# Optimization experiments

Measured on AMD Instinct MI355X. Metric: run time of the kernel, lower is better.

The kernel has to match this reference:

```python
import jax, jax.numpy as jnp
import numpy as np

NUM_HEADS = 6
KERNEL = 5
EPS = 1e-6


def _neighbor_idx(L, k):
    # NATTEN neighborhood: window start clamped so every query has exactly k neighbors
    starts = jnp.clip(jnp.arange(L) - k // 2, 0, L - k)
    return starts[:, None] + jnp.arange(k)  # [L, k]


def ada_rmsnorm(x, scale, w1, b1, w2, b2):
    # x: [B,C,D,H,W]; RMS over spatial dims, gamma from channel means via small MLP
    rms = jnp.sqrt(jnp.mean(x * x, axis=(2, 3, 4), keepdims=True) + EPS)
    xn = x / rms
    stats = jnp.mean(x, axis=(2, 3, 4))                 # [B,C]
    h = jax.nn.relu(stats @ w1.T + b1)                  # [B,2C]
    gamma = jax.nn.sigmoid(h @ w2.T + b2)               # [B,C]
    return xn * (scale * gamma[:, :, None, None, None])


def reference(x, scale1, n1_w1, n1_b1, n1_w2, n1_b2,
              qkv_w, qkv_b, proj_w, proj_b,
              scale2, n2_w1, n2_b1, n2_w2, n2_b2,
              mlp_w1, mlp_b1, mlp_w2, mlp_b2):
    B, C, D, H, W = x.shape
    nh_, k_ = NUM_HEADS, KERNEL
    hd = C // nh_
    K3 = k_ ** 3

    # --- norm1 + neighborhood attention ---
    h = ada_rmsnorm(x, scale1, n1_w1, n1_b1, n1_w2, n1_b2)
    t = jnp.transpose(h, (0, 2, 3, 4, 1))               # [B,D,H,W,C]
    qkv = t @ qkv_w.T + qkv_b                           # [B,D,H,W,3C]
    q, k, v = jnp.split(qkv, 3, axis=-1)
    q = q.reshape(B, D, H, W, nh_, hd)
    k = k.reshape(B, D, H, W, nh_, hd)
    v = v.reshape(B, D, H, W, nh_, hd)

    iD = _neighbor_idx(D, k_)
    iH = _neighbor_idx(H, k_)
    iW = _neighbor_idx(W, k_)
    nd = iD[:, None, None, :, None, None]               # [D,1,1,k,1,1]
    nhh = iH[None, :, None, None, :, None]              # [1,H,1,1,k,1]
    nw = iW[None, None, :, None, None, :]               # [1,1,W,1,1,k]

    k_nb = k[:, nd, nhh, nw].reshape(B, D, H, W, K3, nh_, hd)
    v_nb = v[:, nd, nhh, nw].reshape(B, D, H, W, K3, nh_, hd)

    scale_qk = hd ** -0.5
    scores = jnp.einsum('bdhwnc,bdhwknc->bdhwnk', q, k_nb) * scale_qk  # [B,D,H,W,heads,K3]
    p = jax.nn.softmax(scores, axis=-1)
    o = jnp.einsum('bdhwnk,bdhwknc->bdhwnc', p, v_nb).reshape(B, D, H, W, C)
    o = o @ proj_w.T + proj_b                            # output projection
    x = x + jnp.transpose(o, (0, 4, 1, 2, 3))

    # --- norm2 + 1x1-conv MLP (GELU exact) ---
    h2 = ada_rmsnorm(x, scale2, n2_w1, n2_b1, n2_w2, n2_b2)
    m = jnp.einsum('oc,bcdhw->bodhw', mlp_w1, h2) + mlp_b1[None, :, None, None, None]
    m = jax.nn.gelu(m, approximate=False)
    m = jnp.einsum('oc,bcdhw->bodhw', mlp_w2, m) + mlp_b2[None, :, None, None, None]
    return x + m


def setup_inputs() -> dict:
    key = jax.random.key(0)
    ks = jax.random.split(key, 16)
    B, C, D, H, W = 1, 192, 16, 16, 16
    hid = 2 * C
    mlp_h = int(4.0 * C)
    s = 0.02
    inp = {
        'x': jax.random.normal(ks[0], (B, C, D, H, W), jnp.float32),
        'scale1': jnp.ones((1, C, 1, 1, 1), jnp.float32),
        'n1_w1': jax.random.normal(ks[1], (hid, C), jnp.float32) * s,
        'n1_b1': jnp.zeros((hid,), jnp.float32),
        'n1_w2': jax.random.normal(ks[2], (C, hid), jnp.float32) * s,
        'n1_b2': jnp.zeros((C,), jnp.float32),
        'qkv_w': jax.random.normal(ks[3], (3 * C, C), jnp.float32) * s,
        'qkv_b': jnp.zeros((3 * C,), jnp.float32),
        'proj_w': jax.random.normal(ks[4], (C, C), jnp.float32) * s,
        'proj_b': jnp.zeros((C,), jnp.float32),
        'scale2': jnp.ones((1, C, 1, 1, 1), jnp.float32),
        'n2_w1': jax.random.normal(ks[5], (hid, C), jnp.float32) * s,
        'n2_b1': jnp.zeros((hid,), jnp.float32),
        'n2_w2': jax.random.normal(ks[6], (C, hid), jnp.float32) * s,
        'n2_b2': jnp.zeros((C,), jnp.float32),
        'mlp_w1': jax.random.normal(ks[7], (mlp_h, C), jnp.float32) * s,
        'mlp_b1': jnp.zeros((mlp_h,), jnp.float32),
        'mlp_w2': jax.random.normal(ks[8], (C, mlp_h), jnp.float32) * s,
        'mlp_b2': jnp.zeros((C,), jnp.float32),
    }
    return inp
```

## Files before the change

### kernel.cpp

```cpp
#include <hip/hip_runtime.h>
#include <hip/hip_bf16.h>
#include <cmath>


#define NPOS 4096
#define C_CH 192
#define NB   512

typedef __bf16 bf16x8 __attribute__((ext_vector_type(8)));
typedef __bf16 bf16x4 __attribute__((ext_vector_type(4)));
typedef float  f32x4  __attribute__((ext_vector_type(4)));

__device__ __forceinline__ void pre_sync(unsigned* bar, int grp) {
    __syncthreads();
    if (threadIdx.x == 0) {
        unsigned* arr    = bar + 128 + grp * 16;
        unsigned* master = bar + 256;
        unsigned* go     = bar + 272 + grp * 16;
        unsigned prev = __hip_atomic_fetch_add(arr, 1u, __ATOMIC_RELAXED,
                                               __HIP_MEMORY_SCOPE_AGENT);
        if (prev == 63u) {
            __hip_atomic_fetch_add(master, 1u, __ATOMIC_RELAXED,
                                   __HIP_MEMORY_SCOPE_AGENT);
            while (__hip_atomic_load(master, __ATOMIC_RELAXED,
                                     __HIP_MEMORY_SCOPE_AGENT) < 8u)
                __builtin_amdgcn_s_sleep(2);
            __hip_atomic_store(go, 1u, __ATOMIC_RELAXED, __HIP_MEMORY_SCOPE_AGENT);
        }
        while (__hip_atomic_load(go, __ATOMIC_RELAXED,
                                 __HIP_MEMORY_SCOPE_AGENT) == 0u)
            __builtin_amdgcn_s_sleep(2);
    }
    __syncthreads();
}

__device__ __forceinline__ void grid_sync(unsigned* bar, int idx, int xcc,
                                          unsigned myPop, unsigned nx) {
    __syncthreads();
    if (threadIdx.x == 0) {
        unsigned* base   = bar + 512 + idx * 512;
        unsigned* arr    = base + xcc * 16;
        unsigned* master = base + 128;
        unsigned* go     = base + 144 + xcc * 16;
        unsigned prev = __hip_atomic_fetch_add(arr, 1u, __ATOMIC_RELAXED,
                                               __HIP_MEMORY_SCOPE_AGENT);
        if (prev == myPop - 1u) {
            __hip_atomic_fetch_add(master, 1u, __ATOMIC_RELEASE,
                                   __HIP_MEMORY_SCOPE_AGENT);
            while (__hip_atomic_load(master, __ATOMIC_RELAXED,
                                     __HIP_MEMORY_SCOPE_AGENT) < nx)
                __builtin_amdgcn_s_sleep(2);
            __hip_atomic_store(go, 1u, __ATOMIC_RELAXED, __HIP_MEMORY_SCOPE_AGENT);
        }
        while (__hip_atomic_load(go, __ATOMIC_RELAXED,
                                 __HIP_MEMORY_SCOPE_AGENT) == 0u)
            __builtin_amdgcn_s_sleep(2);
    }
    __syncthreads();
}

__device__ __forceinline__ void conv_unit(const float* __restrict__ src,
                                          __bf16* __restrict__ dst, int base)
{
    int i = (base * 256 + (int)threadIdx.x) * 4;
    float4 v = *(const float4*)(src + i);
    bf16x4 o = { (__bf16)v.x, (__bf16)v.y, (__bf16)v.z, (__bf16)v.w };
    *(bf16x4*)(dst + i) = o;
}

__device__ void stats_unit(float* sm, const float* __restrict__ x,
                           float* __restrict__ sums, float* __restrict__ sumsq, int c)
{
    const float4* xc = (const float4*)(x + (size_t)c * NPOS);
    float a = 0.f, a2 = 0.f;
    for (int i = threadIdx.x; i < NPOS / 4; i += 256) {
        float4 v = xc[i];
        a  += v.x + v.y + v.z + v.w;
        a2 += v.x * v.x + v.y * v.y + v.z * v.z + v.w * v.w;
    }
    #pragma unroll
    for (int off = 32; off > 0; off >>= 1) {
        a  += __shfl_down(a, off);
        a2 += __shfl_down(a2, off);
    }
    float* ls = sm; float* ls2 = sm + 4;
    int wid = threadIdx.x >> 6;
    if ((threadIdx.x & 63) == 0) { ls[wid] = a; ls2[wid] = a2; }
    __syncthreads();
    if (threadIdx.x == 0) {
        float t = 0.f, t2 = 0.f;
        #pragma unroll
        for (int w = 0; w < 4; w++) { t += ls[w]; t2 += ls2[w]; }
        sums[c] = t; sumsq[c] = t2;
    }
    __syncthreads();
}

__device__ void transpose_unit(float* sm, const float* __restrict__ x,
                               __bf16* __restrict__ xb, int p0)
{
    float* lds = sm;
    int t = threadIdx.x;
    for (int idx = t; idx < 192 * 4; idx += 256) {
        int row = idx >> 2, p4 = idx & 3;
        float4 v = *(const float4*)(x + (size_t)row * NPOS + p0 + p4 * 4);
        lds[row * 17 + p4 * 4 + 0] = v.x;
        lds[row * 17 + p4 * 4 + 1] = v.y;
        lds[row * 17 + p4 * 4 + 2] = v.z;
        lds[row * 17 + p4 * 4 + 3] = v.w;
    }
    __syncthreads();
    for (int idx = t; idx < 48 * 16; idx += 256) {
        int c4 = idx >> 4, p = idx & 15;
        bf16x4 o;
        #pragma unroll
        for (int j = 0; j < 4; j++) o[j] = (__bf16)lds[(c4 * 4 + j) * 17 + p];
        *(bf16x4*)(xb + (size_t)(p0 + p) * 192 + c4 * 4) = o;
    }
    __syncthreads();
}

__device__ void compute_gsl(float* scratch, float* gslOut,
    const float* __restrict__ sums, const float* __restrict__ sumsq,
    const float* __restrict__ scale,
    const __bf16* __restrict__ w1b, const float* __restrict__ b1,
    const __bf16* __restrict__ w2b, const float* __restrict__ b2)
{
    float* stats = scratch;
    float* h     = scratch + 192;
    int t = threadIdx.x;
    if (t < C_CH)
        stats[t] = __hip_atomic_load((const float*)&sums[t], __ATOMIC_RELAXED,
                                     __HIP_MEMORY_SCOPE_AGENT) * (1.0f / (float)NPOS);
    __syncthreads();
    for (int j = t; j < 384; j += 256) {
        float acc = b1[j];
        const __bf16* wr = w1b + (size_t)j * C_CH;
        #pragma unroll 4
        for (int c = 0; c < C_CH; c += 8) {
            bf16x8 w8 = *(const bf16x8*)(wr + c);
            acc += (float)w8[0] * stats[c]     + (float)w8[1] * stats[c + 1]
                 + (float)w8[2] * stats[c + 2] + (float)w8[3] * stats[c + 3]
                 + (float)w8[4] * stats[c + 4] + (float)w8[5] * stats[c + 5]
                 + (float)w8[6] * stats[c + 6] + (float)w8[7] * stats[c + 7];
        }
        h[j] = fmaxf(acc, 0.0f);
    }
    __syncthreads();
    if (t < C_CH) {
        float acc = b2[t];
        const __bf16* wr = w2b + (size_t)t * 384;
        #pragma unroll 4
        for (int j = 0; j < 384; j += 8) {
            bf16x8 w8 = *(const bf16x8*)(wr + j);
            acc += (float)w8[0] * h[j]     + (float)w8[1] * h[j + 1]
                 + (float)w8[2] * h[j + 2] + (float)w8[3] * h[j + 3]
                 + (float)w8[4] * h[j + 4] + (float)w8[5] * h[j + 5]
                 + (float)w8[6] * h[j + 6] + (float)w8[7] * h[j + 7];
        }
        float g = 1.0f / (1.0f + __expf(-acc));
        float sq = __hip_atomic_load((const float*)&sumsq[t], __ATOMIC_RELAXED,
                                     __HIP_MEMORY_SCOPE_AGENT);
        float rms = sqrtf(sq * (1.0f / (float)NPOS) + 1e-6f);
        gslOut[t] = scale[t] * g / rms;
    }
    __syncthreads();
}

template <int K, int EPI, bool SCALEA>
__device__ void gemm_tile(__bf16* al, __bf16* bl, const float* gslLds,
    int bx, int by,
    const __bf16* __restrict__ W, const float* __restrict__ bias,
    const __bf16* __restrict__ X, void* __restrict__ out,
    const float* __restrict__ resid, int M, __bf16* __restrict__ out_kv,
    float* __restrict__ s2sum, float* __restrict__ s2sq,
    __bf16* __restrict__ xb2o)
{
    constexpr int KC  = 192;
    constexpr int LDA = 200;
    int t    = threadIdx.x;
    int lane = t & 63;
    int wv   = t >> 6;
    int r16  = lane & 15;
    int quad = lane >> 4;
    int wvm  = wv >> 1;
    int wvn  = wv & 1;
    int mBase = by * 64;
    int nBase = bx * 64;

    f32x4 acc[2][2];
    #pragma unroll
    for (int i = 0; i < 2; i++)
        #pragma unroll
        for (int j = 0; j < 2; j++)
            acc[i][j] = (f32x4){0.f, 0.f, 0.f, 0.f};

    for (int k0 = 0; k0 < K; k0 += KC) {
        #pragma unroll
        for (int it = 0; it < 6; it++) {
            int c = it * 256 + t;
            int row = c / 24, off = c - row * 24;
            bf16x8 va = *(const bf16x8*)(W + (size_t)(mBase + row) * K + k0 + off * 8);
            if (SCALEA) {
                #pragma unroll
                for (int j = 0; j < 8; j++)
                    va[j] = (__bf16)((float)va[j] * gslLds[off * 8 + j]);
            }
            *(bf16x8*)(al + row * LDA + off * 8) = va;
            bf16x8 vb = *(const bf16x8*)(X + (size_t)(nBase + row) * K + k0 + off * 8);
            *(bf16x8*)(bl + row * LDA + off * 8) = vb;
        }
        __syncthreads();
        #pragma unroll
        for (int ks = 0; ks < KC / 32; ks++) {
            bf16x8 a0 = *(const bf16x8*)(al + (wvm * 32 + r16) * LDA + ks * 32 + quad * 8);
            bf16x8 a1 = *(const bf16x8*)(al + (wvm * 32 + 16 + r16) * LDA + ks * 32 + quad * 8);
            bf16x8 b0 = *(const bf16x8*)(bl + (wvn * 32 + r16) * LDA + ks * 32 + quad * 8);
            bf16x8 b1 = *(const bf16x8*)(bl + (wvn * 32 + 16 + r16) * LDA + ks * 32 + quad * 8);
            acc[0][0] = __builtin_amdgcn_mfma_f32_16x16x32_bf16(a0, b0, acc[0][0], 0, 0, 0);
            acc[0][1] = __builtin_amdgcn_mfma_f32_16x16x32_bf16(a0, b1, acc[0][1], 0, 0, 0);
            acc[1][0] = __builtin_amdgcn_mfma_f32_16x16x32_bf16(a1, b0, acc[1][0], 0, 0, 0);
            acc[1][1] = __builtin_amdgcn_mfma_f32_16x16x32_bf16(a1, b1, acc[1][1], 0, 0, 0);
        }
        __syncthreads();
    }

    #pragma unroll
    for (int rt = 0; rt < 2; rt++) {
        int m0 = mBase + wvm * 32 + rt * 16 + quad * 4;
        float b0 = bias[m0], b1v = bias[m0 + 1], b2v = bias[m0 + 2], b3v = bias[m0 + 3];
        float ss[4] = {0.f, 0.f, 0.f, 0.f}, sq[4] = {0.f, 0.f, 0.f, 0.f};
        #pragma unroll
        for (int ct = 0; ct < 2; ct++) {
            int n = nBase + wvn * 32 + ct * 16 + r16;
            f32x4 a4 = acc[rt][ct];
            float g0 = a4[0] + b0, g1 = a4[1] + b1v, g2 = a4[2] + b2v, g3 = a4[3] + b3v;
            if (EPI == 0) {
                int sect = m0 / 192;
                int o0 = m0 - sect * 192;
                if (sect == 0) {
                    const float qs = 0.17677669529663687f;
                    *(float4*)((float*)out + (size_t)n * 192 + o0) =
                        make_float4(g0 * qs, g1 * qs, g2 * qs, g3 * qs);
                } else {
                    bf16x4 kvv = { (__bf16)g0, (__bf16)g1, (__bf16)g2, (__bf16)g3 };
                    *(bf16x4*)(out_kv + (size_t)n * 384 + (o0 >> 2) * 8 + (sect - 1) * 4) = kvv;
                }
            } else if (EPI == 2 || EPI == 4) {
                float* o = (float*)out;
                size_t i0 = (size_t)m0 * NPOS + n;
                float v0 = g0 + resid[i0];
                float v1 = g1 + resid[i0 + NPOS];
                float v2 = g2 + resid[i0 + 2 * NPOS];
                float v3 = g3 + resid[i0 + 3 * NPOS];
                o[i0] = v0; o[i0 + NPOS] = v1; o[i0 + 2 * NPOS] = v2; o[i0 + 3 * NPOS] = v3;
                if (EPI == 4) {
                    bf16x4 xv = { (__bf16)v0, (__bf16)v1, (__bf16)v2, (__bf16)v3 };
                    *(bf16x4*)(xb2o + (size_t)n * 192 + m0) = xv;
                    ss[0] += v0; sq[0] += v0 * v0;
                    ss[1] += v1; sq[1] += v1 * v1;
                    ss[2] += v2; sq[2] += v2 * v2;
                    ss[3] += v3; sq[3] += v3 * v3;
                }
            } else {
                bf16x4 v;
                v[0] = (__bf16)(0.5f * g0 * (1.0f + erff(g0 * 0.7071067811865475f)));
                v[1] = (__bf16)(0.5f * g1 * (1.0f + erff(g1 * 0.7071067811865475f)));
                v[2] = (__bf16)(0.5f * g2 * (1.0f + erff(g2 * 0.7071067811865475f)));
                v[3] = (__bf16)(0.5f * g3 * (1.0f + erff(g3 * 0.7071067811865475f)));
                *(bf16x4*)((__bf16*)out + (size_t)n * M + m0) = v;
            }
        }
        if (EPI == 4) {
            #pragma unroll
            for (int j = 0; j < 4; j++) {
                float s = ss[j], s2v = sq[j];
                #pragma unroll
                for (int off = 8; off >= 1; off >>= 1) {
                    s   += __shfl_down(s, off);
                    s2v += __shfl_down(s2v, off);
                }
                if (r16 == 0) {
                    atomicAdd(&s2sum[m0 + j], s);
                    atomicAdd(&s2sq[m0 + j], s2v);
                }
            }
        }
    }
}

__device__ void attn_mfma(char* smbase, const float* __restrict__ q,
                          const __bf16* __restrict__ kv, __bf16* __restrict__ o,
                          int pb, int head)
{
    __bf16* Qs = (__bf16*)smbase;
    __bf16* Ks = Qs + 64 * 40;
    __bf16* Vt = Ks + 128 * 40;
    __bf16* Ps = Vt + 32 * 136;

    int t = threadIdx.x;
    int wave = t >> 6, lane = t & 63, r16 = lane & 15, quad = lane >> 4;

    int Db = (pb >> 4) * 4, Hb = ((pb >> 2) & 3) * 4, Wb = (pb & 3) * 4;
    int r0d = min(max(Db - 2, 0), 8);
    int r0h = min(max(Hb - 2, 0), 8);
    int r0w = min(max(Wb - 2, 0), 8);

    for (int idx = t; idx < 512; idx += 256) {
        int qr = idx >> 3, c4 = (idx & 7) * 4;
        int pos = (Db + (qr >> 4)) * 256 + (Hb + ((qr >> 2) & 3)) * 16 + (Wb + (qr & 3));
        float4 v = *(const float4*)(q + (size_t)pos * 192 + head * 32 + c4);
        bf16x4 b = { (__bf16)v.x, (__bf16)v.y, (__bf16)v.z, (__bf16)v.w };
        *(bf16x4*)(Qs + qr * 40 + c4) = b;
    }

    int d0q = min(max(Db + wave - 2, 0), 11);
    int h0q = min(max(Hb + quad - 2, 0), 11);
    unsigned wm[4];
    #pragma unroll
    for (int reg = 0; reg < 4; reg++) {
        int w0q = min(max(Wb + reg - 2, 0), 11);
        unsigned m = 0;
        #pragma unroll
        for (int wk = 0; wk < 8; wk++) {
            int wa = r0w + wk;
            if (wa >= w0q && wa < w0q + 5) m |= (1u << wk);
        }
        wm[reg] = m;
    }

    float lpart[4] = {0.f, 0.f, 0.f, 0.f};
    f32x4 accO[2] = { (f32x4){0.f,0.f,0.f,0.f}, (f32x4){0.f,0.f,0.f,0.f} };
    int rowbase = wave * 16;

    for (int c = 0; c < 4; c++) {
        __syncthreads();
        for (int idx = t; idx < 1024; idx += 256) {
            int l128 = idx >> 3, cp = idx & 7;
            int pos = (r0d + c * 2 + (l128 >> 6)) * 256
                    + (r0h + ((l128 >> 3) & 7)) * 16 + (r0w + (l128 & 7));
            uint4 u = *(const uint4*)(kv + (size_t)pos * 384 + head * 64 + cp * 8);
            uint2 kk; kk.x = u.x; kk.y = u.y;
            *(uint2*)(Ks + l128 * 40 + cp * 4) = kk;
            unsigned short* vt0 = (unsigned short*)(Vt + (cp * 4) * 136 + l128);
            vt0[0]         = (unsigned short)(u.z & 0xffff);
            vt0[136]       = (unsigned short)(u.z >> 16);
            vt0[272]       = (unsigned short)(u.w & 0xffff);
            vt0[408]       = (unsigned short)(u.w >> 16);
        }
        __syncthreads();
        bf16x8 aq = *(const bf16x8*)(Qs + (rowbase + r16) * 40 + quad * 8);
        #pragma unroll
        for (int tn = 0; tn < 8; tn++) {
            bf16x8 bk = *(const bf16x8*)(Ks + (tn * 16 + r16) * 40 + quad * 8);
            f32x4 sc = __builtin_amdgcn_mfma_f32_16x16x32_bf16(
                           aq, bk, (f32x4){0.f,0.f,0.f,0.f}, 0, 0, 0);
            int local = tn * 16 + r16;
            int dka = r0d + c * 2 + (local >> 6);
            int hka = r0h + ((local >> 3) & 7);
            int wk  = local & 7;
            bool vdh = (dka >= d0q) && (dka < d0q + 5) &&
                       (hka >= h0q) && (hka < h0q + 5);
            #pragma unroll
            for (int reg = 0; reg < 4; reg++) {
                bool v = vdh && ((wm[reg] >> wk) & 1u);
                float p = v ? __expf(sc[reg]) : 0.f;
                lpart[reg] += p;
                Ps[(rowbase + quad * 4 + reg) * 136 + local] = (__bf16)p;
            }
        }
        __syncthreads();
        #pragma unroll
        for (int tn = 0; tn < 2; tn++) {
            #pragma unroll
            for (int ks = 0; ks < 4; ks++) {
                bf16x8 pa = *(const bf16x8*)(Ps + (rowbase + r16) * 136 + ks * 32 + quad * 8);
                bf16x8 bv = *(const bf16x8*)(Vt + (tn * 16 + r16) * 136 + ks * 32 + quad * 8);
                accO[tn] = __builtin_amdgcn_mfma_f32_16x16x32_bf16(pa, bv, accO[tn], 0, 0, 0);
            }
        }
    }

    #pragma unroll
    for (int reg = 0; reg < 4; reg++) {
        #pragma unroll
        for (int off = 1; off < 16; off <<= 1)
            lpart[reg] += __shfl_xor(lpart[reg], off);
    }
    #pragma unroll
    for (int tn = 0; tn < 2; tn++) {
        #pragma unroll
        for (int reg = 0; reg < 4; reg++) {
            int qr = rowbase + quad * 4 + reg;
            int pos = (Db + (qr >> 4)) * 256 + (Hb + ((qr >> 2) & 3)) * 16 + (Wb + (qr & 3));
            o[(size_t)pos * 192 + head * 32 + tn * 16 + r16] =
                (__bf16)(accO[tn][reg] / lpart[reg]);
        }
    }
}

__global__ __launch_bounds__(256) void fused(
    const float* __restrict__ x, const float* __restrict__ scale1,
    const float* __restrict__ n1_w1, const float* __restrict__ n1_b1,
    const float* __restrict__ n1_w2, const float* __restrict__ n1_b2,
    const float* __restrict__ qkv_w, const float* __restrict__ qkv_b,
    const float* __restrict__ proj_w, const float* __restrict__ proj_b,
    const float* __restrict__ scale2,
    const float* __restrict__ n2_w1, const float* __restrict__ n2_b1,
    const float* __restrict__ n2_w2, const float* __restrict__ n2_b2,
    const float* __restrict__ mlp_w1, const float* __restrict__ mlp_b1,
    const float* __restrict__ mlp_w2, const float* __restrict__ mlp_b2,
    float* __restrict__ ws, float* __restrict__ x2)
{
    __shared__ __align__(16) char smraw[52224];
    __bf16* al     = (__bf16*)smraw;
    __bf16* bl     = al + 64 * 200;
    float*  smf    = (float*)smraw;
    float*  gslLds = (float*)(smraw + 51200);

    float*  q_buf   = ws;
    __bf16* kv_buf  = (__bf16*)(ws + 786432);
    __bf16* xb      = (__bf16*)(ws + 2359296);
    __bf16* o_attn  = (__bf16*)(ws + 2752512);
    __bf16* qkv_wb  = (__bf16*)(ws + 3145728);
    __bf16* proj_wb = qkv_wb + 110592;
    __bf16* m1_wb   = proj_wb + 36864;
    __bf16* m2_wb   = m1_wb + 147456;
    float*  sums1   = ws + 3366912;
    float*  sumsq1  = ws + 3367104;
    float*  sums2   = ws + 3367296;
    float*  sumsq2  = ws + 3367488;
    __bf16* n1w1b   = (__bf16*)(ws + 3367680);
    __bf16* n1w2b   = n1w1b + 73728;
    __bf16* n2w1b   = n1w2b + 73728;
    __bf16* n2w2b   = n2w1b + 73728;
    unsigned* bar   = (unsigned*)(ws + 3515136);
    __bf16* m_buf   = (__bf16*)(ws + 3520512);
    __bf16* xb2     = (__bf16*)(ws + 5093376);

    int bid = blockIdx.x;
    int t   = threadIdx.x;

    int xcc = __builtin_amdgcn_s_getreg(63508) & 7;

    if (t == 0)
        __hip_atomic_fetch_add(bar + xcc * 16, 1u, __ATOMIC_RELAXED,
                               __HIP_MEMORY_SCOPE_AGENT);
    pre_sync(bar, bid & 7);
    unsigned myPop = 0, nx = 0;
    if (t == 0) {
        myPop = __hip_atomic_load(bar + xcc * 16, __ATOMIC_RELAXED,
                                  __HIP_MEMORY_SCOPE_AGENT);
        #pragma unroll
        for (int xi = 0; xi < 8; xi++)
            nx += (__hip_atomic_load(bar + xi * 16, __ATOMIC_RELAXED,
                                     __HIP_MEMORY_SCOPE_AGENT) > 0u) ? 1u : 0u;
    }

    for (int u = bid; u < 1169; u += NB) {
        if      (u < 108)  conv_unit(qkv_w,  qkv_wb, u);
        else if (u < 144)  conv_unit(proj_w, proj_wb, u - 108);
        else if (u < 288)  conv_unit(mlp_w1, m1_wb, u - 144);
        else if (u < 432)  conv_unit(mlp_w2, m2_wb, u - 288);
        else if (u < 504)  conv_unit(n1_w1,  n1w1b, u - 432);
        else if (u < 576)  conv_unit(n1_w2,  n1w2b, u - 504);
        else if (u < 648)  conv_unit(n2_w1,  n2w1b, u - 576);
        else if (u < 720)  conv_unit(n2_w2,  n2w2b, u - 648);
        else if (u < 912)  stats_unit(smf, x, sums1, sumsq1, u - 720);
        else if (u == 912) {
            if (t < 192) {
                __hip_atomic_store(&sums2[t], 0.f, __ATOMIC_RELAXED,
                                   __HIP_MEMORY_SCOPE_AGENT);
                __hip_atomic_store(&sumsq2[t], 0.f, __ATOMIC_RELAXED,
                                   __HIP_MEMORY_SCOPE_AGENT);
            }
        }
        else               transpose_unit(smf, x, xb, (u - 913) * 16);
    }
    grid_sync(bar, 0, xcc, myPop, nx);

    compute_gsl(smf, gslLds, sums1, sumsq1, scale1, n1w1b, n1_b1, n1w2b, n1_b2);
    for (int tile = bid; tile < 576; tile += NB)
        gemm_tile<192, 0, true>(al, bl, gslLds, tile & 63, tile >> 6,
                                qkv_wb, qkv_b, xb, (void*)q_buf,
                                nullptr, 576, kv_buf, nullptr, nullptr, nullptr);
    grid_sync(bar, 1, xcc, myPop, nx);

    if (bid < 384)
        attn_mfma(smraw, q_buf, kv_buf, o_attn, bid / 6, bid % 6);
    grid_sync(bar, 2, xcc, myPop, nx);

    if (bid < 192)
        gemm_tile<192, 4, false>(al, bl, nullptr, bid & 63, bid >> 6,
                                 proj_wb, proj_b, o_attn, (void*)x2,
                                 x, 192, nullptr, sums2, sumsq2, xb2);
    grid_sync(bar, 3, xcc, myPop, nx);

    compute_gsl(smf, gslLds, sums2, sumsq2, scale2, n2w1b, n2_b1, n2w2b, n2_b2);
    for (int tile = bid; tile < 768; tile += NB)
        gemm_tile<192, 3, true>(al, bl, gslLds, tile & 63, tile >> 6,
                                m1_wb, mlp_b1, xb2, (void*)m_buf,
                                nullptr, 768, nullptr, nullptr, nullptr, nullptr);
    grid_sync(bar, 4, xcc, myPop, nx);

    if (bid < 192)
        gemm_tile<768, 2, false>(al, bl, nullptr, bid & 63, bid >> 6,
                                 m2_wb, mlp_b2, m_buf, (void*)x2,
                                 x2, 192, nullptr, nullptr, nullptr, nullptr);
}

extern "C" void kernel_launch(void* const* d_in, const int* in_sizes, int n_in,
                              void* d_out, int out_size, void* d_ws, size_t ws_size,
                              hipStream_t stream)
{
    const float* x      = (const float*)d_in[0];
    const float* scale1 = (const float*)d_in[1];
    const float* n1_w1  = (const float*)d_in[2];
    const float* n1_b1  = (const float*)d_in[3];
    const float* n1_w2  = (const float*)d_in[4];
    const float* n1_b2  = (const float*)d_in[5];
    const float* qkv_w  = (const float*)d_in[6];
    const float* qkv_b  = (const float*)d_in[7];
    const float* proj_w = (const float*)d_in[8];
    const float* proj_b = (const float*)d_in[9];
    const float* scale2 = (const float*)d_in[10];
    const float* n2_w1  = (const float*)d_in[11];
    const float* n2_b1  = (const float*)d_in[12];
    const float* n2_w2  = (const float*)d_in[13];
    const float* n2_b2  = (const float*)d_in[14];
    const float* mlp_w1 = (const float*)d_in[15];
    const float* mlp_b1 = (const float*)d_in[16];
    const float* mlp_w2 = (const float*)d_in[17];
    const float* mlp_b2 = (const float*)d_in[18];

    float* ws = (float*)d_ws;
    float* x2 = (float*)d_out;

    hipMemsetAsync(ws + 3515136, 0, 3072 * sizeof(unsigned), stream);

    fused<<<NB, 256, 0, stream>>>(x, scale1, n1_w1, n1_b1, n1_w2, n1_b2,
                                  qkv_w, qkv_b, proj_w, proj_b,
                                  scale2, n2_w1, n2_b1, n2_w2, n2_b2,
                                  mlp_w1, mlp_b1, mlp_w2, mlp_b2,
                                  ws, x2);
}
```

Measured before the change: 192.8 us.

## Fuse RMS stats into transpose pass and grow persistent grid to 768 blocks

Result: slower. 213.5 us (+10.7%).

```diff
diff --git a/kernel.cpp b/kernel.cpp
--- a/kernel.cpp
+++ b/kernel.cpp
@@ -5,7 +5,7 @@
 
 #define NPOS 4096
 #define C_CH 192
-#define NB   512
+#define NB   768
 
 typedef __bf16 bf16x8 __attribute__((ext_vector_type(8)));
 typedef __bf16 bf16x4 __attribute__((ext_vector_type(4)));
@@ -19,7 +19,7 @@
         unsigned* go     = bar + 272 + grp * 16;
         unsigned prev = __hip_atomic_fetch_add(arr, 1u, __ATOMIC_RELAXED,
                                                __HIP_MEMORY_SCOPE_AGENT);
-        if (prev == 63u) {
+        if (prev == (NB / 8 - 1)) {
             __hip_atomic_fetch_add(master, 1u, __ATOMIC_RELAXED,
                                    __HIP_MEMORY_SCOPE_AGENT);
             while (__hip_atomic_load(master, __ATOMIC_RELAXED,
@@ -68,36 +68,10 @@
     *(bf16x4*)(dst + i) = o;
 }
 
-__device__ void stats_unit(float* sm, const float* __restrict__ x,
-                           float* __restrict__ sums, float* __restrict__ sumsq, int c)
-{
-    const float4* xc = (const float4*)(x + (size_t)c * NPOS);
-    float a = 0.f, a2 = 0.f;
-    for (int i = threadIdx.x; i < NPOS / 4; i += 256) {
-        float4 v = xc[i];
-        a  += v.x + v.y + v.z + v.w;
-        a2 += v.x * v.x + v.y * v.y + v.z * v.z + v.w * v.w;
-    }
-    #pragma unroll
-    for (int off = 32; off > 0; off >>= 1) {
-        a  += __shfl_down(a, off);
-        a2 += __shfl_down(a2, off);
-    }
-    float* ls = sm; float* ls2 = sm + 4;
-    int wid = threadIdx.x >> 6;
-    if ((threadIdx.x & 63) == 0) { ls[wid] = a; ls2[wid] = a2; }
-    __syncthreads();
-    if (threadIdx.x == 0) {
-        float t = 0.f, t2 = 0.f;
-        #pragma unroll
-        for (int w = 0; w < 4; w++) { t += ls[w]; t2 += ls2[w]; }
-        sums[c] = t; sumsq[c] = t2;
-    }
-    __syncthreads();
-}
-
-__device__ void transpose_unit(float* sm, const float* __restrict__ x,
-                               __bf16* __restrict__ xb, int p0)
+__device__ void transpose_stats_unit(float* sm, const float* __restrict__ x,
+                                     __bf16* __restrict__ xb, int p0,
+                                     float* __restrict__ sums,
+                                     float* __restrict__ sumsq)
 {
     float* lds = sm;
     int t = threadIdx.x;
@@ -108,6 +82,14 @@
         lds[row * 17 + p4 * 4 + 1] = v.y;
         lds[row * 17 + p4 * 4 + 2] = v.z;
         lds[row * 17 + p4 * 4 + 3] = v.w;
+        float s  = v.x + v.y + v.z + v.w;
+        float s2 = v.x * v.x + v.y * v.y + v.z * v.z + v.w * v.w;
+        s  += __shfl_xor(s, 1);  s  += __shfl_xor(s, 2);
+        s2 += __shfl_xor(s2, 1); s2 += __shfl_xor(s2, 2);
+        if ((t & 3) == 0) {
+            atomicAdd(&sums[row], s);
+            atomicAdd(&sumsq[row], s2);
+        }
     }
     __syncthreads();
     for (int idx = t; idx < 48 * 16; idx += 256) {
@@ -343,10 +325,10 @@
             uint2 kk; kk.x = u.x; kk.y = u.y;
             *(uint2*)(Ks + l128 * 40 + cp * 4) = kk;
             unsigned short* vt0 = (unsigned short*)(Vt + (cp * 4) * 136 + l128);
-            vt0[0]         = (unsigned short)(u.z & 0xffff);
-            vt0[136]       = (unsigned short)(u.z >> 16);
-            vt0[272]       = (unsigned short)(u.w & 0xffff);
-            vt0[408]       = (unsigned short)(u.w >> 16);
+            vt0[0]   = (unsigned short)(u.z & 0xffff);
+            vt0[136] = (unsigned short)(u.z >> 16);
+            vt0[272] = (unsigned short)(u.w & 0xffff);
+            vt0[408] = (unsigned short)(u.w >> 16);
         }
         __syncthreads();
         bf16x8 aq = *(const bf16x8*)(Qs + (rowbase + r16) * 40 + quad * 8);
@@ -426,15 +408,15 @@
     __bf16* proj_wb = qkv_wb + 110592;
     __bf16* m1_wb   = proj_wb + 36864;
     __bf16* m2_wb   = m1_wb + 147456;
-    float*  sums1   = ws + 3366912;
-    float*  sumsq1  = ws + 3367104;
-    float*  sums2   = ws + 3367296;
-    float*  sumsq2  = ws + 3367488;
     __bf16* n1w1b   = (__bf16*)(ws + 3367680);
     __bf16* n1w2b   = n1w1b + 73728;
     __bf16* n2w1b   = n1w2b + 73728;
     __bf16* n2w2b   = n2w1b + 73728;
     unsigned* bar   = (unsigned*)(ws + 3515136);
+    float*  sums1   = ws + 3518208;
+    float*  sumsq1  = ws + 3518400;
+    float*  sums2   = ws + 3518592;
+    float*  sumsq2  = ws + 3518784;
     __bf16* m_buf   = (__bf16*)(ws + 3520512);
     __bf16* xb2     = (__bf16*)(ws + 5093376);
 
@@ -457,7 +439,7 @@
                                      __HIP_MEMORY_SCOPE_AGENT) > 0u) ? 1u : 0u;
     }
 
-    for (int u = bid; u < 1169; u += NB) {
+    for (int u = bid; u < 976; u += NB) {
         if      (u < 108)  conv_unit(qkv_w,  qkv_wb, u);
         else if (u < 144)  conv_unit(proj_w, proj_wb, u - 108);
         else if (u < 288)  conv_unit(mlp_w1, m1_wb, u - 144);
@@ -466,16 +448,8 @@
         else if (u < 576)  conv_unit(n1_w2,  n1w2b, u - 504);
         else if (u < 648)  conv_unit(n2_w1,  n2w1b, u - 576);
         else if (u < 720)  conv_unit(n2_w2,  n2w2b, u - 648);
-        else if (u < 912)  stats_unit(smf, x, sums1, sumsq1, u - 720);
-        else if (u == 912) {
-            if (t < 192) {
-                __hip_atomic_store(&sums2[t], 0.f, __ATOMIC_RELAXED,
-                                   __HIP_MEMORY_SCOPE_AGENT);
-                __hip_atomic_store(&sumsq2[t], 0.f, __ATOMIC_RELAXED,
-                                   __HIP_MEMORY_SCOPE_AGENT);
-            }
-        }
-        else               transpose_unit(smf, x, xb, (u - 913) * 16);
+        else               transpose_stats_unit(smf, x, xb, (u - 720) * 16,
+                                                sums1, sumsq1);
     }
     grid_sync(bar, 0, xcc, myPop, nx);
 
@@ -536,7 +510,7 @@
     float* ws = (float*)d_ws;
     float* x2 = (float*)d_out;
 
-    hipMemsetAsync(ws + 3515136, 0, 3072 * sizeof(unsigned), stream);
+    hipMemsetAsync(ws + 3515136, 0, 3840 * sizeof(unsigned), stream);
 
     fused<<<NB, 256, 0, stream>>>(x, scale1, n1_w1, n1_b1, n1_w2, n1_b2,
                                   qkv_w, qkv_b, proj_w, proj_b,
```
